# Kernel tuning notes

Measured on AMD Instinct MI355X. Metric: run time of the kernel, lower is better.

Reference implementation:

```python
import jax, jax.numpy as jnp
import numpy as np

N_NODES = 100000
N_EDGES = 3200000
D_FEAT = 512
HIDDEN = 16
N_CLASSES = 7


def _gcn_conv(x, W, b, src, dst, n_nodes):
    """PyG GCNConv (add_self_loops=True, normalize=True):
    out = D^{-1/2} (A + I) D^{-1/2} X W + b, aggregated at target nodes (dst).
    src/dst already include self loops."""
    h = x @ W  # [N, out_dim] -- transform before scatter (small message dim)
    ones = jnp.ones(dst.shape[0], dtype=x.dtype)
    deg = jax.ops.segment_sum(ones, dst, num_segments=n_nodes)  # in-degree incl. self loop
    dinv = jnp.where(deg > 0, jax.lax.rsqrt(deg), 0.0)
    norm = dinv[src] * dinv[dst]  # [E_tot]
    msg = h[src] * norm[:, None]  # gather + scale
    out = jax.ops.segment_sum(msg, dst, num_segments=n_nodes)  # scatter-add
    return out + b


def setup_inputs() -> dict:
    key = jax.random.key(0)
    k1, k2, k3, k4 = jax.random.split(key, 4)
    x = jax.random.normal(k1, (N_NODES, D_FEAT), dtype=jnp.float32)
    edge_index = jax.random.randint(k2, (2, N_EDGES), 0, N_NODES, dtype=jnp.int64)
    # Glorot-ish init for weights
    W1 = jax.random.normal(k3, (D_FEAT, HIDDEN), dtype=jnp.float32) / np.sqrt(D_FEAT)
    b1 = jnp.zeros((HIDDEN,), dtype=jnp.float32)
    W2 = jax.random.normal(k4, (HIDDEN, N_CLASSES), dtype=jnp.float32) / np.sqrt(HIDDEN)
    b2 = jnp.zeros((N_CLASSES,), dtype=jnp.float32)
    return {"x": x, "edge_index": edge_index, "W1": W1, "b1": b1, "W2": W2, "b2": b2}


def reference(x, edge_index, W1, b1, W2, b2):
    n = x.shape[0]
    loop = jnp.arange(n, dtype=edge_index.dtype)
    src = jnp.concatenate([edge_index[0], loop])  # add self loops (fixed shape)
    dst = jnp.concatenate([edge_index[1], loop])
    h = _gcn_conv(x, W1, b1, src, dst, n)
    h = jax.nn.relu(h)
    # F.dropout(training=self.training): identity in eval/inference baseline
    h = _gcn_conv(h, W2, b2, src, dst, n)
    return jax.nn.log_softmax(h, axis=1)
```

## Files before the change

### kernel.cpp

```cpp
#include <hip/hip_runtime.h>

#define NN 100000
#define NE 3200000
#define DF 512
#define HID 16
#define NC 7
#define NBK 782
#define BCAP 6144
#define GEMM_BLOCKS 782
#define SC_B 640
#define SEDG 5000

__global__ void k_zero_i(int* __restrict__ p, int n) {
    int i = blockIdx.x * blockDim.x + threadIdx.x;
    if (i < n) p[i] = 0;
}

union SMem {
    float w[DF * HID];
    struct {
        int stage[SEDG];
        int off[783];
        int part[512];
        int cur[782];
        int gofs[782];
    } s;
};

__global__ __launch_bounds__(512) void k_fused(const float* __restrict__ x,
                                               const float* __restrict__ W1,
                                               const int* __restrict__ src,
                                               const int* __restrict__ dst,
                                               float* __restrict__ h1,
                                               int* __restrict__ bcnt,
                                               int* __restrict__ pk) {
    __shared__ SMem u;
    int tid = threadIdx.x;
    if (blockIdx.x < SC_B) {
        int* stage = u.s.stage;
        int* off   = u.s.off;
        int* part  = u.s.part;
        int* cur   = u.s.cur;
        int* gofs  = u.s.gofs;
        int e0 = blockIdx.x * SEDG;
        for (int i = tid; i < NBK; i += 512) cur[i] = 0;
        __syncthreads();
        for (int e = e0 + tid; e < e0 + SEDG; e += 512) atomicAdd(&cur[dst[e] >> 7], 1);
        __syncthreads();
        {
            int base = tid * 2;
            int sum = 0;
#pragma unroll
            for (int j = 0; j < 2; ++j) if (base + j < NBK) sum += cur[base + j];
            part[tid] = sum;
            __syncthreads();
            for (int s2 = 1; s2 < 512; s2 <<= 1) {
                int v = (tid >= s2) ? part[tid - s2] : 0;
                __syncthreads();
                part[tid] += v;
                __syncthreads();
            }
            int run = (tid > 0) ? part[tid - 1] : 0;
#pragma unroll
            for (int j = 0; j < 2; ++j) {
                int idx = base + j;
                if (idx < NBK) { off[idx] = run; run += cur[idx]; }
            }
            if (tid == 0) off[NBK] = SEDG;
        }
        __syncthreads();
        for (int i = tid; i < NBK; i += 512) {
            int h = cur[i];
            int g = h ? atomicAdd(&bcnt[i], h) : 0;
            gofs[i] = g - off[i];
            cur[i] = off[i];
        }
        __syncthreads();
        for (int e = e0 + tid; e < e0 + SEDG; e += 512) {
            int d = dst[e];
            int pos = atomicAdd(&cur[d >> 7], 1);
            stage[pos] = src[e] | ((d & 127) << 17);
        }
        __syncthreads();
        for (int i = tid; i < SEDG; i += 512) {
            int lo = 0, hi = NBK;
            while (hi - lo > 1) { int mid = (lo + hi) >> 1; if (off[mid] <= i) lo = mid; else hi = mid; }
            int idx = gofs[lo] + i;
            if (idx < BCAP) pk[(size_t)lo * BCAP + idx] = stage[i];
        }
        return;
    }
    {
        const float4* wg = (const float4*)W1;
        float4* wl = (float4*)u.w;
#pragma unroll
        for (int i = 0; i < 4; ++i) wl[tid + 512 * i] = wg[tid + 512 * i];
    }
    __syncthreads();
    int wid = (blockIdx.x - SC_B) * 8 + (tid >> 6);
    int lane = tid & 63;
    int r = lane >> 2, cc = lane & 3;
    int row = wid * 16 + r;
    if (row >= NN) return;
    const float4* xr = (const float4*)(x + (size_t)row * DF);
    const float4* wl = (const float4*)u.w;
    float4 acc = make_float4(0.f, 0.f, 0.f, 0.f);
#pragma unroll 8
    for (int i = 0; i < DF / 4; ++i) {
        float4 xv = xr[i];
        float4 w0 = wl[(4 * i + 0) * 4 + cc];
        float4 w1v = wl[(4 * i + 1) * 4 + cc];
        float4 w2 = wl[(4 * i + 2) * 4 + cc];
        float4 w3 = wl[(4 * i + 3) * 4 + cc];
        acc.x = fmaf(xv.x, w0.x, fmaf(xv.y, w1v.x, fmaf(xv.z, w2.x, fmaf(xv.w, w3.x, acc.x))));
        acc.y = fmaf(xv.x, w0.y, fmaf(xv.y, w1v.y, fmaf(xv.z, w2.y, fmaf(xv.w, w3.y, acc.y))));
        acc.z = fmaf(xv.x, w0.z, fmaf(xv.y, w1v.z, fmaf(xv.z, w2.z, fmaf(xv.w, w3.z, acc.z))));
        acc.w = fmaf(xv.x, w0.w, fmaf(xv.y, w1v.w, fmaf(xv.z, w2.w, fmaf(xv.w, w3.w, acc.w))));
    }
    *(float4*)(h1 + (size_t)row * HID + cc * 4) = acc;
}

__global__ __launch_bounds__(256) void k_sortB(const int* __restrict__ bcnt,
                                               int* __restrict__ pk,
                                               float* __restrict__ dinv,
                                               float* __restrict__ h1,
                                               int* __restrict__ ptrg,
                                               int* __restrict__ cntg) {
    __shared__ int sorted[BCAP];
    __shared__ int hist[128];
    __shared__ int off[128];
    __shared__ int cur[128];
    __shared__ float dl[128];
    int b = blockIdx.x, tid = threadIdx.x;
    if (tid < 128) hist[tid] = 0;
    __syncthreads();
    int n = min(bcnt[b], BCAP);
    int* p = pk + (size_t)b * BCAP;
    for (int i = tid; i < n; i += 256) atomicAdd(&hist[p[i] >> 17], 1);
    __syncthreads();
    if (tid < 128) off[tid] = hist[tid];
    __syncthreads();
    for (int s2 = 1; s2 < 128; s2 <<= 1) {
        int u = 0;
        if (tid < 128 && tid >= s2) u = off[tid - s2];
        __syncthreads();
        if (tid < 128) off[tid] += u;
        __syncthreads();
    }
    if (tid < 128) {
        int start = off[tid] - hist[tid];
        cur[tid] = start;
        int node = b * 128 + tid;
        float di = rsqrtf((float)hist[tid] + 1.0f);
        dl[tid] = di;
        if (node < NN) {
            dinv[node] = di;
            ptrg[node] = b * BCAP + start;
            cntg[node] = hist[tid];
        }
    }
    __syncthreads();
    for (int i = tid; i < n; i += 256) {
        int v = p[i];
        int pos = atomicAdd(&cur[v >> 17], 1);
        sorted[pos] = v & 0x1FFFF;
    }
    __syncthreads();
    for (int i = tid; i < n; i += 256) p[i] = sorted[i];
    float4* hp = (float4*)(h1 + (size_t)b * 128 * HID);
    for (int i = tid; i < 512; i += 256) {
        int ln = i >> 2;
        int node = b * 128 + ln;
        if (node < NN) {
            float di = dl[ln];
            float4 v = hp[i];
            v.x *= di; v.y *= di; v.z *= di; v.w *= di;
            hp[i] = v;
        }
    }
}

__global__ __launch_bounds__(256) void k_agg1(const int* __restrict__ ptrg,
                                              const int* __restrict__ cntg,
                                              const int* __restrict__ csr,
                                              const float* __restrict__ dinv,
                                              const float* __restrict__ h1s,
                                              const float* __restrict__ b1,
                                              const float* __restrict__ W2,
                                              float* __restrict__ h2s) {
    int tid = threadIdx.x;
    int ch = tid & 15;
    int d = blockIdx.x * 16 + (tid >> 4);
    if (d >= NN) return;
    int st = ptrg[d], n = cntg[d];
    float did = dinv[d];
    float a0 = 0.f, a1 = 0.f;
    int e = st, end = st + n;
    for (; e + 1 < end; e += 2) {
        int s0 = csr[e], s1 = csr[e + 1];
        a0 += h1s[(size_t)s0 * HID + ch];
        a1 += h1s[(size_t)s1 * HID + ch];
    }
    if (e < end) a0 += h1s[(size_t)csr[e] * HID + ch];
    float acc = (a0 + a1 + h1s[(size_t)d * HID + ch]) * did + b1[ch];
    float hr = fmaxf(acc, 0.f);
    float hj = 0.f;
#pragma unroll
    for (int k = 0; k < HID; ++k) {
        float hk = __shfl(hr, k, 16);
        if (ch < NC) hj = fmaf(hk, W2[k * NC + ch], hj);
    }
    if (ch < NC) h2s[(size_t)d * NC + ch] = hj * did;
}

__global__ __launch_bounds__(256) void k_agg2(const int* __restrict__ ptrg,
                                              const int* __restrict__ cntg,
                                              const int* __restrict__ csr,
                                              const float* __restrict__ dinv,
                                              const float* __restrict__ h2s,
                                              const float* __restrict__ b2,
                                              float* __restrict__ out) {
    int tid = threadIdx.x;
    int ch = tid & 7;
    int d = blockIdx.x * 32 + (tid >> 3);
    if (d >= NN) return;
    int st = ptrg[d], n = cntg[d];
    float did = dinv[d];
    float a0 = 0.f, a1 = 0.f;
    int e = st, end = st + n;
    for (; e + 1 < end; e += 2) {
        int s0 = csr[e], s1 = csr[e + 1];
        if (ch < NC) {
            a0 += h2s[(size_t)s0 * NC + ch];
            a1 += h2s[(size_t)s1 * NC + ch];
        }
    }
    if (e < end && ch < NC) a0 += h2s[(size_t)csr[e] * NC + ch];
    float o = -1e30f;
    if (ch < NC) o = (a0 + a1 + h2s[(size_t)d * NC + ch]) * did + b2[ch];
    float m = o;
#pragma unroll
    for (int offm = 1; offm < 8; offm <<= 1) m = fmaxf(m, __shfl_xor(m, offm, 8));
    float ex = (ch < NC) ? expf(o - m) : 0.f;
    float s8 = ex;
#pragma unroll
    for (int offm = 1; offm < 8; offm <<= 1) s8 += __shfl_xor(s8, offm, 8);
    if (ch < NC) out[(size_t)d * NC + ch] = o - m - logf(s8);
}

extern "C" void kernel_launch(void* const* d_in, const int* in_sizes, int n_in,
                              void* d_out, int out_size, void* d_ws, size_t ws_size,
                              hipStream_t stream) {
    const float* x  = (const float*)d_in[0];
    const int*   ei = (const int*)d_in[1];
    const float* W1 = (const float*)d_in[2];
    const float* b1 = (const float*)d_in[3];
    const float* W2 = (const float*)d_in[4];
    const float* b2 = (const float*)d_in[5];
    float* out = (float*)d_out;

    const int* src = ei;
    const int* dst = ei + NE;

    int*   bcnt = (int*)d_ws;
    int*   pk   = bcnt + 784;
    float* dinv = (float*)(pk + (size_t)NBK * BCAP);
    float* h1   = dinv + NN;
    float* h2   = h1 + (size_t)HID * NN;
    int*   ptrg = (int*)(h2 + (size_t)NC * NN);
    int*   cntg = ptrg + NN;

    k_zero_i<<<4, 256, 0, stream>>>(bcnt, 784);
    k_fused <<<SC_B + GEMM_BLOCKS, 512, 0, stream>>>(x, W1, src, dst, h1, bcnt, pk);
    k_sortB <<<NBK, 256, 0, stream>>>(bcnt, pk, dinv, h1, ptrg, cntg);
    k_agg1  <<<(NN + 15) / 16, 256, 0, stream>>>(ptrg, cntg, pk, dinv, h1, b1, W2, h2);
    k_agg2  <<<(NN + 31) / 32, 256, 0, stream>>>(ptrg, cntg, pk, dinv, h2, b2, out);
}
```

Before: 193.1 us.

## Split fused scatter/GEMM kernel and pipeline GEMM x loads through LDS

Separates the edge-bucketing scatter and the X·W1 GEMM into two kernels, so they no longer share one launch. The GEMM now stages x rows into swizzled LDS double buffers with async global_load_lds and computes two rows per thread, aiming to overlap memory with compute and raise bandwidth use on the 200MB x read. The cost is that the two phases no longer run concurrently in one launch and an extra launch is added.

```diff
diff --git a/kernel.cpp b/kernel.cpp
--- a/kernel.cpp
+++ b/kernel.cpp
@@ -7,117 +7,141 @@
 #define NC 7
 #define NBK 782
 #define BCAP 6144
-#define GEMM_BLOCKS 782
 #define SC_B 640
 #define SEDG 5000
+#define GB 782
 
 __global__ void k_zero_i(int* __restrict__ p, int n) {
     int i = blockIdx.x * blockDim.x + threadIdx.x;
     if (i < n) p[i] = 0;
 }
 
-union SMem {
-    float w[DF * HID];
-    struct {
-        int stage[SEDG];
-        int off[783];
-        int part[512];
-        int cur[782];
-        int gofs[782];
-    } s;
-};
-
-__global__ __launch_bounds__(512) void k_fused(const float* __restrict__ x,
-                                               const float* __restrict__ W1,
-                                               const int* __restrict__ src,
-                                               const int* __restrict__ dst,
-                                               float* __restrict__ h1,
-                                               int* __restrict__ bcnt,
-                                               int* __restrict__ pk) {
-    __shared__ SMem u;
+__global__ __launch_bounds__(512) void k_scat(const int* __restrict__ src,
+                                              const int* __restrict__ dst,
+                                              int* __restrict__ bcnt,
+                                              int* __restrict__ pk) {
+    __shared__ int stage[SEDG];
+    __shared__ int off[NBK + 1];
+    __shared__ int part[512];
+    __shared__ int cur[NBK];
+    __shared__ int gofs[NBK];
     int tid = threadIdx.x;
-    if (blockIdx.x < SC_B) {
-        int* stage = u.s.stage;
-        int* off   = u.s.off;
-        int* part  = u.s.part;
-        int* cur   = u.s.cur;
-        int* gofs  = u.s.gofs;
-        int e0 = blockIdx.x * SEDG;
-        for (int i = tid; i < NBK; i += 512) cur[i] = 0;
+    int e0 = blockIdx.x * SEDG;
+    for (int i = tid; i < NBK; i += 512) cur[i] = 0;
+    __syncthreads();
+    for (int e = e0 + tid; e < e0 + SEDG; e += 512) atomicAdd(&cur[dst[e] >> 7], 1);
+    __syncthreads();
+    {
+        int base = tid * 2;
+        int sum = 0;
+#pragma unroll
+        for (int j = 0; j < 2; ++j) if (base + j < NBK) sum += cur[base + j];
+        part[tid] = sum;
         __syncthreads();
-        for (int e = e0 + tid; e < e0 + SEDG; e += 512) atomicAdd(&cur[dst[e] >> 7], 1);
-        __syncthreads();
-        {
-            int base = tid * 2;
-            int sum = 0;
-#pragma unroll
-            for (int j = 0; j < 2; ++j) if (base + j < NBK) sum += cur[base + j];
-            part[tid] = sum;
+        for (int s2 = 1; s2 < 512; s2 <<= 1) {
+            int v = (tid >= s2) ? part[tid - s2] : 0;
             __syncthreads();
-            for (int s2 = 1; s2 < 512; s2 <<= 1) {
-                int v = (tid >= s2) ? part[tid - s2] : 0;
-                __syncthreads();
-                part[tid] += v;
-                __syncthreads();
-            }
-            int run = (tid > 0) ? part[tid - 1] : 0;
-#pragma unroll
-            for (int j = 0; j < 2; ++j) {
-                int idx = base + j;
-                if (idx < NBK) { off[idx] = run; run += cur[idx]; }
-            }
-            if (tid == 0) off[NBK] = SEDG;
-        }
-        __syncthreads();
-        for (int i = tid; i < NBK; i += 512) {
-            int h = cur[i];
-            int g = h ? atomicAdd(&bcnt[i], h) : 0;
-            gofs[i] = g - off[i];
-            cur[i] = off[i];
-        }
-        __syncthreads();
-        for (int e = e0 + tid; e < e0 + SEDG; e += 512) {
-            int d = dst[e];
-            int pos = atomicAdd(&cur[d >> 7], 1);
-            stage[pos] = src[e] | ((d & 127) << 17);
-        }
-        __syncthreads();
-        for (int i = tid; i < SEDG; i += 512) {
-            int lo = 0, hi = NBK;
-            while (hi - lo > 1) { int mid = (lo + hi) >> 1; if (off[mid] <= i) lo = mid; else hi = mid; }
-            int idx = gofs[lo] + i;
-            if (idx < BCAP) pk[(size_t)lo * BCAP + idx] = stage[i];
-        }
-        return;
-    }
+            part[tid] += v;
+            __syncthreads();
+        }
+        int run = (tid > 0) ? part[tid - 1] : 0;
+#pragma unroll
+        for (int j = 0; j < 2; ++j) {
+            int idx = base + j;
+            if (idx < NBK) { off[idx] = run; run += cur[idx]; }
+        }
+        if (tid == 0) off[NBK] = SEDG;
+    }
+    __syncthreads();
+    for (int i = tid; i < NBK; i += 512) {
+        int h = cur[i];
+        int g = h ? atomicAdd(&bcnt[i], h) : 0;
+        gofs[i] = g - off[i];
+        cur[i] = off[i];
+    }
+    __syncthreads();
+    for (int e = e0 + tid; e < e0 + SEDG; e += 512) {
+        int d = dst[e];
+        int pos = atomicAdd(&cur[d >> 7], 1);
+        stage[pos] = src[e] | ((d & 127) << 17);
+    }
+    __syncthreads();
+    for (int i = tid; i < SEDG; i += 512) {
+        int lo = 0, hi = NBK;
+        while (hi - lo > 1) { int mid = (lo + hi) >> 1; if (off[mid] <= i) lo = mid; else hi = mid; }
+        int idx = gofs[lo] + i;
+        if (idx < BCAP) pk[(size_t)lo * BCAP + idx] = stage[i];
+    }
+}
+
+__global__ __launch_bounds__(256) void k_gemm(const float* __restrict__ x,
+                                              const float* __restrict__ W1,
+                                              float* __restrict__ h1) {
+    __shared__ float4 wb[2048];
+    __shared__ float4 xb[4][2][256];
+    int tid = threadIdx.x;
     {
         const float4* wg = (const float4*)W1;
-        float4* wl = (float4*)u.w;
-#pragma unroll
-        for (int i = 0; i < 4; ++i) wl[tid + 512 * i] = wg[tid + 512 * i];
-    }
-    __syncthreads();
-    int wid = (blockIdx.x - SC_B) * 8 + (tid >> 6);
+#pragma unroll
+        for (int i = 0; i < 8; ++i) wb[tid + 256 * i] = wg[tid + 256 * i];
+    }
+    __syncthreads();
+    int wid = tid >> 6;
     int lane = tid & 63;
     int r = lane >> 2, cc = lane & 3;
-    int row = wid * 16 + r;
-    if (row >= NN) return;
-    const float4* xr = (const float4*)(x + (size_t)row * DF);
-    const float4* wl = (const float4*)u.w;
-    float4 acc = make_float4(0.f, 0.f, 0.f, 0.f);
-#pragma unroll 8
-    for (int i = 0; i < DF / 4; ++i) {
-        float4 xv = xr[i];
-        float4 w0 = wl[(4 * i + 0) * 4 + cc];
-        float4 w1v = wl[(4 * i + 1) * 4 + cc];
-        float4 w2 = wl[(4 * i + 2) * 4 + cc];
-        float4 w3 = wl[(4 * i + 3) * 4 + cc];
-        acc.x = fmaf(xv.x, w0.x, fmaf(xv.y, w1v.x, fmaf(xv.z, w2.x, fmaf(xv.w, w3.x, acc.x))));
-        acc.y = fmaf(xv.x, w0.y, fmaf(xv.y, w1v.y, fmaf(xv.z, w2.y, fmaf(xv.w, w3.y, acc.y))));
-        acc.z = fmaf(xv.x, w0.z, fmaf(xv.y, w1v.z, fmaf(xv.z, w2.z, fmaf(xv.w, w3.z, acc.z))));
-        acc.w = fmaf(xv.x, w0.w, fmaf(xv.y, w1v.w, fmaf(xv.z, w2.w, fmaf(xv.w, w3.w, acc.w))));
-    }
-    *(float4*)(h1 + (size_t)row * HID + cc * 4) = acc;
+    int row_base = blockIdx.x * 128 + wid * 32;
+    int s_rl7 = (lane >> 3) & 7;
+    int s_j = lane & 7;
+    int s_k4 = s_j ^ s_rl7;
+    long srow0 = row_base + (lane >> 3);
+#define STAGE(hb, c)                                                            \
+    {                                                                           \
+        _Pragma("unroll")                                                       \
+        for (int t = 0; t < 4; ++t) {                                           \
+            long rr = srow0 + t * 8;                                            \
+            if (rr >= NN) rr = NN - 1;                                          \
+            const float* gsrc = x + rr * DF + (c) * 32 + s_k4 * 4;              \
+            float4* ldst = &xb[wid][hb][t * 64];                                \
+            __builtin_amdgcn_global_load_lds(                                   \
+                (const __attribute__((address_space(1))) void*)gsrc,            \
+                (__attribute__((address_space(3))) void*)ldst, 16, 0, 0);       \
+        }                                                                       \
+    }
+    float4 acc0 = make_float4(0.f, 0.f, 0.f, 0.f);
+    float4 acc1 = make_float4(0.f, 0.f, 0.f, 0.f);
+    int r7 = r & 7;
+    STAGE(0, 0);
+    for (int c = 0; c < 16; ++c) {
+        int hb = c & 1;
+        if (c < 15) STAGE(hb ^ 1, c + 1);
+        if (c < 15) asm volatile("s_waitcnt vmcnt(4)" ::: "memory");
+        else        asm volatile("s_waitcnt vmcnt(0)" ::: "memory");
+        __builtin_amdgcn_sched_barrier(0);
+        const float4* xw = xb[wid][hb];
+#pragma unroll
+        for (int i = 0; i < 8; ++i) {
+            float4 xv0 = xw[r * 8 + (i ^ r7)];
+            float4 xv1 = xw[(r + 16) * 8 + (i ^ r7)];
+            int kq = c * 8 + i;
+            float4 w0 = wb[(4 * kq + 0) * 4 + cc];
+            float4 w1v = wb[(4 * kq + 1) * 4 + cc];
+            float4 w2 = wb[(4 * kq + 2) * 4 + cc];
+            float4 w3 = wb[(4 * kq + 3) * 4 + cc];
+            acc0.x = fmaf(xv0.x, w0.x, fmaf(xv0.y, w1v.x, fmaf(xv0.z, w2.x, fmaf(xv0.w, w3.x, acc0.x))));
+            acc0.y = fmaf(xv0.x, w0.y, fmaf(xv0.y, w1v.y, fmaf(xv0.z, w2.y, fmaf(xv0.w, w3.y, acc0.y))));
+            acc0.z = fmaf(xv0.x, w0.z, fmaf(xv0.y, w1v.z, fmaf(xv0.z, w2.z, fmaf(xv0.w, w3.z, acc0.z))));
+            acc0.w = fmaf(xv0.x, w0.w, fmaf(xv0.y, w1v.w, fmaf(xv0.z, w2.w, fmaf(xv0.w, w3.w, acc0.w))));
+            acc1.x = fmaf(xv1.x, w0.x, fmaf(xv1.y, w1v.x, fmaf(xv1.z, w2.x, fmaf(xv1.w, w3.x, acc1.x))));
+            acc1.y = fmaf(xv1.x, w0.y, fmaf(xv1.y, w1v.y, fmaf(xv1.z, w2.y, fmaf(xv1.w, w3.y, acc1.y))));
+            acc1.z = fmaf(xv1.x, w0.z, fmaf(xv1.y, w1v.z, fmaf(xv1.z, w2.z, fmaf(xv1.w, w3.z, acc1.z))));
+            acc1.w = fmaf(xv1.x, w0.w, fmaf(xv1.y, w1v.w, fmaf(xv1.z, w2.w, fmaf(xv1.w, w3.w, acc1.w))));
+        }
+    }
+    long row0 = row_base + r;
+    long row1 = row_base + 16 + r;
+    if (row0 < NN) *(float4*)(h1 + row0 * HID + cc * 4) = acc0;
+    if (row1 < NN) *(float4*)(h1 + row1 * HID + cc * 4) = acc1;
+#undef STAGE
 }
 
 __global__ __launch_bounds__(256) void k_sortB(const int* __restrict__ bcnt,
@@ -271,7 +295,8 @@
     int*   cntg = ptrg + NN;
 
     k_zero_i<<<4, 256, 0, stream>>>(bcnt, 784);
-    k_fused <<<SC_B + GEMM_BLOCKS, 512, 0, stream>>>(x, W1, src, dst, h1, bcnt, pk);
+    k_scat  <<<SC_B, 512, 0, stream>>>(src, dst, bcnt, pk);
+    k_gemm  <<<GB, 256, 0, stream>>>(x, W1, h1);
     k_sortB <<<NBK, 256, 0, stream>>>(bcnt, pk, dinv, h1, ptrg, cntg);
     k_agg1  <<<(NN + 15) / 16, 256, 0, stream>>>(ptrg, cntg, pk, dinv, h1, b1, W2, h2);
     k_agg2  <<<(NN + 31) / 32, 256, 0, stream>>>(ptrg, cntg, pk, dinv, h2, b2, out);
```

After: 199.4 us. +3.2%, slower.

## Stage X rows into LDS with async global_load_lds double buffering in GEMM

Applied to the files above, without the earlier changes.

The x@W1 part of the fused kernel now has each wave compute 32 rows instead of 16 and loads X tiles through direct global-to-LDS async loads into a double buffer, waiting on vmcnt. This halves the number of GEMM blocks and lets each wave reuse W1 LDS reads across two rows. The intent is coalesced, overlapped streaming of the 200MB X matrix in place of strided per-thread float4 loads. It adds LDS footprint and relies on hand-written waitcnt and sched_barrier ordering.

```diff
diff --git a/kernel.cpp b/kernel.cpp
--- a/kernel.cpp
+++ b/kernel.cpp
@@ -7,9 +7,9 @@
 #define NC 7
 #define NBK 782
 #define BCAP 6144
-#define GEMM_BLOCKS 782
 #define SC_B 640
 #define SEDG 5000
+#define GB 391
 
 __global__ void k_zero_i(int* __restrict__ p, int n) {
     int i = blockIdx.x * blockDim.x + threadIdx.x;
@@ -17,13 +17,16 @@
 }
 
 union SMem {
-    float w[DF * HID];
+    struct {
+        float4 wb[2048];
+        float4 xb[8][2][128];
+    } g;
     struct {
         int stage[SEDG];
-        int off[783];
+        int off[NBK + 1];
         int part[512];
-        int cur[782];
-        int gofs[782];
+        int cur[NBK];
+        int gofs[NBK];
     } s;
 };
 
@@ -92,32 +95,68 @@
     }
     {
         const float4* wg = (const float4*)W1;
-        float4* wl = (float4*)u.w;
-#pragma unroll
-        for (int i = 0; i < 4; ++i) wl[tid + 512 * i] = wg[tid + 512 * i];
-    }
-    __syncthreads();
-    int wid = (blockIdx.x - SC_B) * 8 + (tid >> 6);
+#pragma unroll
+        for (int i = 0; i < 4; ++i) u.g.wb[tid + 512 * i] = wg[tid + 512 * i];
+    }
+    __syncthreads();
+    int gb = blockIdx.x - SC_B;
+    int wid = tid >> 6;
     int lane = tid & 63;
     int r = lane >> 2, cc = lane & 3;
-    int row = wid * 16 + r;
-    if (row >= NN) return;
-    const float4* xr = (const float4*)(x + (size_t)row * DF);
-    const float4* wl = (const float4*)u.w;
-    float4 acc = make_float4(0.f, 0.f, 0.f, 0.f);
-#pragma unroll 8
-    for (int i = 0; i < DF / 4; ++i) {
-        float4 xv = xr[i];
-        float4 w0 = wl[(4 * i + 0) * 4 + cc];
-        float4 w1v = wl[(4 * i + 1) * 4 + cc];
-        float4 w2 = wl[(4 * i + 2) * 4 + cc];
-        float4 w3 = wl[(4 * i + 3) * 4 + cc];
-        acc.x = fmaf(xv.x, w0.x, fmaf(xv.y, w1v.x, fmaf(xv.z, w2.x, fmaf(xv.w, w3.x, acc.x))));
-        acc.y = fmaf(xv.x, w0.y, fmaf(xv.y, w1v.y, fmaf(xv.z, w2.y, fmaf(xv.w, w3.y, acc.y))));
-        acc.z = fmaf(xv.x, w0.z, fmaf(xv.y, w1v.z, fmaf(xv.z, w2.z, fmaf(xv.w, w3.z, acc.z))));
-        acc.w = fmaf(xv.x, w0.w, fmaf(xv.y, w1v.w, fmaf(xv.z, w2.w, fmaf(xv.w, w3.w, acc.w))));
-    }
-    *(float4*)(h1 + (size_t)row * HID + cc * 4) = acc;
+    long row_base = (long)gb * 256 + wid * 32;
+    int srow = lane & 31;
+    int sq = lane >> 5;
+    long grow = row_base + srow;
+    if (grow >= NN) grow = NN - 1;
+    const float* gbase = x + grow * DF + sq * 4;
+#define STAGE(hb, c)                                                            \
+    {                                                                           \
+        _Pragma("unroll")                                                       \
+        for (int t = 0; t < 2; ++t) {                                           \
+            const float* gsrc = gbase + (c) * 16 + t * 8;                       \
+            float4* ldst = &u.g.xb[wid][hb][t * 64];                            \
+            __builtin_amdgcn_global_load_lds(                                   \
+                (const __attribute__((address_space(1))) void*)gsrc,            \
+                (__attribute__((address_space(3))) void*)ldst, 16, 0, 0);       \
+        }                                                                       \
+    }
+    float4 acc0 = make_float4(0.f, 0.f, 0.f, 0.f);
+    float4 acc1 = make_float4(0.f, 0.f, 0.f, 0.f);
+    STAGE(0, 0);
+    for (int c = 0; c < 32; ++c) {
+        int hb = c & 1;
+        if (c < 31) {
+            STAGE(hb ^ 1, c + 1);
+            asm volatile("s_waitcnt vmcnt(2)" ::: "memory");
+        } else {
+            asm volatile("s_waitcnt vmcnt(0)" ::: "memory");
+        }
+        __builtin_amdgcn_sched_barrier(0);
+        const float4* xw = u.g.xb[wid][hb];
+#pragma unroll
+        for (int i = 0; i < 4; ++i) {
+            float4 xv0 = xw[i * 32 + r];
+            float4 xv1 = xw[i * 32 + 16 + r];
+            int kq = c * 4 + i;
+            float4 w0 = u.g.wb[(4 * kq + 0) * 4 + cc];
+            float4 w1v = u.g.wb[(4 * kq + 1) * 4 + cc];
+            float4 w2 = u.g.wb[(4 * kq + 2) * 4 + cc];
+            float4 w3 = u.g.wb[(4 * kq + 3) * 4 + cc];
+            acc0.x = fmaf(xv0.x, w0.x, fmaf(xv0.y, w1v.x, fmaf(xv0.z, w2.x, fmaf(xv0.w, w3.x, acc0.x))));
+            acc0.y = fmaf(xv0.x, w0.y, fmaf(xv0.y, w1v.y, fmaf(xv0.z, w2.y, fmaf(xv0.w, w3.y, acc0.y))));
+            acc0.z = fmaf(xv0.x, w0.z, fmaf(xv0.y, w1v.z, fmaf(xv0.z, w2.z, fmaf(xv0.w, w3.z, acc0.z))));
+            acc0.w = fmaf(xv0.x, w0.w, fmaf(xv0.y, w1v.w, fmaf(xv0.z, w2.w, fmaf(xv0.w, w3.w, acc0.w))));
+            acc1.x = fmaf(xv1.x, w0.x, fmaf(xv1.y, w1v.x, fmaf(xv1.z, w2.x, fmaf(xv1.w, w3.x, acc1.x))));
+            acc1.y = fmaf(xv1.x, w0.y, fmaf(xv1.y, w1v.y, fmaf(xv1.z, w2.y, fmaf(xv1.w, w3.y, acc1.y))));
+            acc1.z = fmaf(xv1.x, w0.z, fmaf(xv1.y, w1v.z, fmaf(xv1.z, w2.z, fmaf(xv1.w, w3.z, acc1.z))));
+            acc1.w = fmaf(xv1.x, w0.w, fmaf(xv1.y, w1v.w, fmaf(xv1.z, w2.w, fmaf(xv1.w, w3.w, acc1.w))));
+        }
+    }
+    long row0 = row_base + r;
+    long row1 = row_base + 16 + r;
+    if (row0 < NN) *(float4*)(h1 + row0 * HID + cc * 4) = acc0;
+    if (row1 < NN) *(float4*)(h1 + row1 * HID + cc * 4) = acc1;
+#undef STAGE
 }
 
 __global__ __launch_bounds__(256) void k_sortB(const int* __restrict__ bcnt,
@@ -271,7 +310,7 @@
     int*   cntg = ptrg + NN;
 
     k_zero_i<<<4, 256, 0, stream>>>(bcnt, 784);
-    k_fused <<<SC_B + GEMM_BLOCKS, 512, 0, stream>>>(x, W1, src, dst, h1, bcnt, pk);
+    k_fused <<<SC_B + GB, 512, 0, stream>>>(x, W1, src, dst, h1, bcnt, pk);
     k_sortB <<<NBK, 256, 0, stream>>>(bcnt, pk, dinv, h1, ptrg, cntg);
     k_agg1  <<<(NN + 15) / 16, 256, 0, stream>>>(ptrg, cntg, pk, dinv, h1, b1, W2, h2);
     k_agg2  <<<(NN + 31) / 32, 256, 0, stream>>>(ptrg, cntg, pk, dinv, h2, b2, out);
```

After: 222.1 us. 15.0% more time.
